# Performance work log

Measured on AMD Instinct MI355X. Metric: run time of the kernel, lower is better.

## Reference

```python
import jax, jax.numpy as jnp
import numpy as np

N, E, D, H, R = 100000, 1600000, 128, 128, 8


def rgcn_layer(x, W_rel, W_root, bias, src, dst, etype):
    """PyG-style RGCNConv: per-relation mean aggregation + root transform.

    out[i] = x[i] @ W_root + bias + sum_r mean_{j: (j->i, r)} x[j] @ W_rel[r]
    Mean commutes with the linear map, so we segment-mean raw features per
    (dst, relation) pair, then apply a single batched einsum.
    """
    n = x.shape[0]
    r = W_rel.shape[0]
    seg = dst * r + etype                                   # [E]
    msg = x[src]                                            # [E, D]
    agg = jax.ops.segment_sum(msg, seg, num_segments=n * r)  # [N*R, D]
    cnt = jax.ops.segment_sum(jnp.ones((msg.shape[0],), x.dtype), seg,
                              num_segments=n * r)
    agg = agg / jnp.maximum(cnt, 1.0)[:, None]              # per-relation mean
    agg = agg.reshape(n, r, -1)                             # [N, R, D]
    return jnp.einsum('nrd,rdh->nh', agg, W_rel) + x @ W_root + bias


def setup_inputs() -> dict:
    key = jax.random.key(0)
    ks = jax.random.split(key, 12)
    x = jax.random.normal(ks[0], (N, D), dtype=jnp.float32)
    edge_index = jax.random.randint(ks[1], (2, E), 0, N, dtype=jnp.int64)
    edge_type = jax.random.randint(ks[2], (E,), 0, R, dtype=jnp.int64)
    s = lambda fan_in: 1.0 / np.sqrt(fan_in)
    W_rel1 = jax.random.normal(ks[3], (R, D, H), dtype=jnp.float32) * s(D)
    W_root1 = jax.random.normal(ks[4], (D, H), dtype=jnp.float32) * s(D)
    b1 = jnp.zeros((H,), dtype=jnp.float32)
    W_rel2 = jax.random.normal(ks[5], (R, H, H), dtype=jnp.float32) * s(H)
    W_root2 = jax.random.normal(ks[6], (H, H), dtype=jnp.float32) * s(H)
    b2 = jnp.zeros((H,), dtype=jnp.float32)
    out_w = jax.random.normal(ks[7], (H, 1), dtype=jnp.float32) * s(H)
    out_b = jnp.zeros((1,), dtype=jnp.float32)
    return {"x": x, "edge_index": edge_index, "edge_type": edge_type,
            "W_rel1": W_rel1, "W_root1": W_root1, "b1": b1,
            "W_rel2": W_rel2, "W_root2": W_root2, "b2": b2,
            "out_w": out_w, "out_b": out_b}


def reference(x, edge_index, edge_type, W_rel1, W_root1, b1,
              W_rel2, W_root2, b2, out_w, out_b):
    src, dst = edge_index[0], edge_index[1]
    h = jax.nn.relu(rgcn_layer(x, W_rel1, W_root1, b1, src, dst, edge_type))
    h = jax.nn.relu(rgcn_layer(h, W_rel2, W_root2, b2, src, dst, edge_type))
    return jax.nn.sigmoid(h @ out_w + out_b).squeeze(-1)  # [N]
```

## Files before the change

### kernel.cpp

```cpp
#include <hip/hip_runtime.h>
#include <cstdint>
#include <cstddef>

#define NNODES 100000
#define NEDGES 1600000
#define DIM 128
#define NREL 8
#define QCAP 40
#define QI4 (QCAP / 4)
#define NKT 36
#define A16ROW 1160
#define NB 196
#define BCAP 9216
#define EPB 8192
#define BIN_BLKS ((NEDGES + EPB - 1) / EPB)
#define CVT4 (NNODES * DIM / 4)
#define CVT_BLKS (CVT4 / 1024)
#define PACK_UNITS (NKT * 8 * 2)
#define PACK_BLKS ((PACK_UNITS + 15) / 16)

typedef float f32x4 __attribute__((ext_vector_type(4)));
typedef float float8 __attribute__((ext_vector_type(8)));
typedef short short8 __attribute__((ext_vector_type(8)));
typedef _Float16 half8 __attribute__((ext_vector_type(8)));

__device__ inline unsigned short f2h(float f) {
    return __builtin_bit_cast(unsigned short, (_Float16)f);
}

__global__ __launch_bounds__(1024) void passA(const int* __restrict__ src,
                                              const int* __restrict__ dst,
                                              const int* __restrict__ et,
                                              int* __restrict__ gcur,
                                              int* __restrict__ qtmp,
                                              const float* __restrict__ x,
                                              unsigned short* __restrict__ xh,
                                              const float* __restrict__ Wrel1,
                                              const float* __restrict__ Wroot1,
                                              const float* __restrict__ Wrel2,
                                              const float* __restrict__ Wroot2,
                                              unsigned short* __restrict__ Wp1,
                                              unsigned short* __restrict__ Wp2) {
    int b = blockIdx.x;
    const int tid = threadIdx.x;
    if (b < BIN_BLKS) {
        __shared__ int cnt[NB];
        __shared__ int cur[NB];
        if (tid < NB) cnt[tid] = 0;
        __syncthreads();
        int ent[8], bkt[8];
        const int ebase = b * EPB + tid;
#pragma unroll
        for (int k = 0; k < 8; ++k) {
            int e = ebase + k * 1024;
            bkt[k] = -1;
            if (e < NEDGES) {
                int d = dst[e];
                int bb = d >> 9;
                bkt[k] = bb;
                ent[k] = src[e] | (et[e] << 17) | ((d & 511) << 20);
                atomicAdd(&cnt[bb], 1);
            }
        }
        __syncthreads();
        if (tid < NB) {
            int c = cnt[tid];
            cur[tid] = (c > 0) ? atomicAdd(&gcur[tid], c) : 0;
        }
        __syncthreads();
#pragma unroll
        for (int k = 0; k < 8; ++k) {
            if (bkt[k] >= 0) {
                int p = atomicAdd(&cur[bkt[k]], 1);
                if (p < BCAP) qtmp[(size_t)bkt[k] * BCAP + p] = ent[k];
            }
        }
        return;
    }
    b -= BIN_BLKS;
    if (b < CVT_BLKS) {
        int gid = b * 1024 + tid;
        float4 v = *(const float4*)(x + (size_t)gid * 4);
        ushort4 o = make_ushort4(f2h(v.x), f2h(v.y), f2h(v.z), f2h(v.w));
        *(ushort4*)(xh + (size_t)gid * 4) = o;
        return;
    }
    b -= CVT_BLKS;
    int unit = b * 16 + (tid >> 6);
    if (unit >= PACK_UNITS) return;
    int lane = tid & 63;
    int bb = unit;
    const float* Wrel = Wrel1;
    const float* Wroot = Wroot1;
    unsigned short* Wp = Wp1;
    if (bb >= NKT * 8) {
        bb -= NKT * 8;
        Wrel = Wrel2; Wroot = Wroot2; Wp = Wp2;
    }
    const int kt = bb >> 3, ht = bb & 7;
    const int col = ht * 16 + (lane & 15);
    const int kbase = kt * 32 + (lane >> 4) * 8;
    unsigned short vals[8];
#pragma unroll
    for (int j = 0; j < 8; ++j) {
        int k = kbase + j;
        float f = (k < 1024) ? Wrel[(size_t)k * 128 + col]
                             : Wroot[(size_t)(k - 1024) * 128 + col];
        vals[j] = f2h(f);
    }
    unsigned short* dstp = Wp + ((size_t)bb * 64 + lane) * 8;
#pragma unroll
    for (int j = 0; j < 8; ++j) dstp[j] = vals[j];
}

__global__ __launch_bounds__(1024) void passB(const int* __restrict__ qtmp,
                                              const int* __restrict__ gcur,
                                              int* __restrict__ fill,
                                              int* __restrict__ qlist) {
    const int b = blockIdx.x;
    const int tid = threadIdx.x;
    __shared__ int ncnt[512];
    if (tid < 512) ncnt[tid] = 0;
    __syncthreads();
    int total = gcur[b];
    if (total > BCAP) total = BCAP;
    int ent[9], loc[9];
#pragma unroll
    for (int k = 0; k < 9; ++k) {
        int i = tid + k * 1024;
        loc[k] = -1;
        if (i < total) {
            int e = qtmp[(size_t)b * BCAP + i];
            ent[k] = e;
            loc[k] = ((unsigned)e) >> 20;
            atomicAdd(&ncnt[loc[k]], 1);
        }
    }
    __syncthreads();
    if (tid < 512) {
        int n = b * 512 + tid;
        if (n < NNODES) fill[n] = ncnt[tid];
        ncnt[tid] = 0;
    }
    __syncthreads();
#pragma unroll
    for (int k = 0; k < 9; ++k) {
        if (loc[k] >= 0) {
            int p = atomicAdd(&ncnt[loc[k]], 1);
            if (p < QCAP) {
                int n = b * 512 + loc[k];
                int cv = (ent[k] & 0x1FFFF) | (((((unsigned)ent[k]) >> 17) & 7) << 20);
                qlist[(size_t)n * QCAP + p] = cv;
            }
        }
    }
}

#define FLUSH8 {                                                               \
    float sc = __shfl(invv, cur, 8);                                           \
    short8 o;                                                                  \
    _Pragma("unroll")                                                          \
    for (int j = 0; j < 8; ++j) o[j] = (short)f2h(accv[j] * sc);               \
    *(short8*)(Arow + cur * DIM + l16 * 8) = o;                                \
    accv = (float8){0.f, 0.f, 0.f, 0.f, 0.f, 0.f, 0.f, 0.f};                   \
}

__global__ __launch_bounds__(512, 4) void fused_layer(
    const unsigned short* __restrict__ feat,
    const int* __restrict__ fill,
    const int* __restrict__ qlist,
    const unsigned short* __restrict__ Wp,
    const float* __restrict__ bias,
    unsigned short* __restrict__ out,
    const float* __restrict__ outw,
    const float* __restrict__ outb,
    float* __restrict__ head_out) {
    __shared__ __align__(16) unsigned short A16[32 * A16ROW + 8];
    __shared__ int qs[32][QCAP];
    __shared__ int cnt[32][8];
    const int tid = threadIdx.x;
    const int blk = blockIdx.x;
    const int g = tid >> 4, l16 = tid & 15;

    const int n = blk * 32 + g;
    const int r8 = l16 & 7;

    const int fraw = fill[n];
    const int ecnt = fraw < QCAP ? fraw : QCAP;

    unsigned short* Arow = &A16[g * A16ROW];

    *(short8*)(Arow + 1024 + l16 * 8) =
        *(const short8*)(feat + (size_t)n * DIM + l16 * 8);

    if (l16 < 8) cnt[g][l16] = 0;
    int4 raw = make_int4(0, 0, 0, 0);
    if (l16 < QI4)
        raw = *(const int4*)(qlist + (size_t)n * QCAP + l16 * 4);
    __builtin_amdgcn_sched_barrier(0);
    {
        int vals[4] = {raw.x, raw.y, raw.z, raw.w};
        const int bidx = l16 * 4;
        if (l16 < QI4) {
#pragma unroll
            for (int j = 0; j < 4; ++j)
                if (bidx + j < ecnt)
                    atomicAdd(&cnt[g][((unsigned)vals[j]) >> 20], 1);
        }
        __builtin_amdgcn_sched_barrier(0);
        const int c = cnt[g][r8];
        const float invv_ = 1.0f / (float)(c > 1 ? c : 1);

#pragma unroll
        for (int r = 0; r < 8; ++r) {
            int cr = __shfl(c, r, 16);
            if (cr == 0) {
                short8 z = {0, 0, 0, 0, 0, 0, 0, 0};
                *(short8*)(Arow + r * DIM + l16 * 8) = z;
            }
        }

        int incl = c;
#pragma unroll
        for (int d1 = 1; d1 < 8; d1 <<= 1) {
            int u = __shfl_up(incl, d1, 8);
            if (r8 >= d1) incl += u;
        }
        if (l16 < 8) cnt[g][l16] = incl - c;
        __builtin_amdgcn_sched_barrier(0);
        if (l16 < QI4) {
#pragma unroll
            for (int j = 0; j < 4; ++j)
                if (bidx + j < ecnt) {
                    int rel = ((unsigned)vals[j]) >> 20;
                    int p = atomicAdd(&cnt[g][rel], 1);
                    qs[g][p] = vals[j];
                }
        }
        __builtin_amdgcn_sched_barrier(0);

        if (ecnt > 0) {
            const float invv = invv_;
            const int last = ecnt - 1;
            int q[8], qn[8];
            short8 v[8];
#pragma unroll
            for (int u = 0; u < 8; ++u) q[u] = qs[g][u < last ? u : last];
#pragma unroll
            for (int u = 0; u < 8; ++u)
                v[u] = *(const short8*)(feat +
                         (size_t)((unsigned)q[u] & 0xFFFFFu) * DIM + l16 * 8);

            float8 accv = {0.f, 0.f, 0.f, 0.f, 0.f, 0.f, 0.f, 0.f};
            int cur = ((unsigned)q[0]) >> 20;

            for (int e = 0; e < ecnt; e += 8) {
#pragma unroll
                for (int u = 0; u < 8; ++u) {
                    int p = e + 8 + u;
                    qn[u] = qs[g][p < last ? p : last];
                }
#pragma unroll
                for (int u = 0; u < 8; ++u) {
                    if (e + u < ecnt) {
                        const int s = ((unsigned)q[u]) >> 20;
                        if (s != cur) { FLUSH8 cur = s; }
                        accv += __builtin_convertvector(
                            __builtin_bit_cast(half8, v[u]), float8);
                    }
                }
#pragma unroll
                for (int u = 0; u < 8; ++u) {
                    v[u] = *(const short8*)(feat +
                             (size_t)((unsigned)qn[u] & 0xFFFFFu) * DIM + l16 * 8);
                    q[u] = qn[u];
                }
            }
            FLUSH8
        }
    }
    __syncthreads();

    const int lane = tid & 63;
    const int w = tid >> 6;
    const int m = lane & 15, kq = lane >> 4;
    const unsigned short* arow0 = &A16[m * A16ROW + kq * 8];
    const unsigned short* arow1 = &A16[(m + 16) * A16ROW + kq * 8];
    const unsigned short* bb = Wp + ((size_t)w * 64 + lane) * 8;

    f32x4 acc0 = {0.f, 0.f, 0.f, 0.f};
    f32x4 acc1 = {0.f, 0.f, 0.f, 0.f};
#pragma unroll 4
    for (int kt = 0; kt < NKT; ++kt) {
        short8 b0 = *(const short8*)(bb + (size_t)kt * 4096);
        short8 a0 = *(const short8*)(arow0 + kt * 32);
        short8 a1 = *(const short8*)(arow1 + kt * 32);
        acc0 = __builtin_amdgcn_mfma_f32_16x16x32_f16(
            __builtin_bit_cast(half8, a0), __builtin_bit_cast(half8, b0), acc0, 0, 0, 0);
        acc1 = __builtin_amdgcn_mfma_f32_16x16x32_f16(
            __builtin_bit_cast(half8, a1), __builtin_bit_cast(half8, b0), acc1, 0, 0, 0);
    }

    const int col = lane & 15;
    const int rbase = kq * 4;
    const int h0 = 16 * w + col;
    const float bv0 = bias[h0];

    if (!head_out) {
#pragma unroll
        for (int r = 0; r < 4; ++r) {
            const size_t nrow0 = ((size_t)blk * 32 + rbase + r) * DIM;
            const size_t nrow1 = ((size_t)blk * 32 + 16 + rbase + r) * DIM;
            out[nrow0 + h0] = f2h(fmaxf(acc0[r] + bv0, 0.f));
            out[nrow1 + h0] = f2h(fmaxf(acc1[r] + bv0, 0.f));
        }
    } else {
        const float w0 = outw[h0];
        float p0[4], p1[4];
#pragma unroll
        for (int r = 0; r < 4; ++r) {
            p0[r] = fmaxf(acc0[r] + bv0, 0.f) * w0;
            p1[r] = fmaxf(acc1[r] + bv0, 0.f) * w0;
#pragma unroll
            for (int d = 1; d < 16; d <<= 1) {
                p0[r] += __shfl_xor(p0[r], d, 16);
                p1[r] += __shfl_xor(p1[r], d, 16);
            }
        }
        __syncthreads();
        float* hp = (float*)A16;
        if (col == 0) {
#pragma unroll
            for (int r = 0; r < 4; ++r) {
                hp[(rbase + r) * 8 + w] = p0[r];
                hp[(16 + rbase + r) * 8 + w] = p1[r];
            }
        }
        __syncthreads();
        if (tid < 32) {
            float vsum = outb[0];
#pragma unroll
            for (int k = 0; k < 8; ++k) vsum += hp[tid * 8 + k];
            head_out[blk * 32 + tid] = 1.0f / (1.0f + __expf(-vsum));
        }
    }
}

extern "C" void kernel_launch(void* const* d_in, const int* in_sizes, int n_in,
                              void* d_out, int out_size, void* d_ws, size_t ws_size,
                              hipStream_t stream) {
    const float* x      = (const float*)d_in[0];
    const int*   ei     = (const int*)d_in[1];
    const int*   et     = (const int*)d_in[2];
    const float* Wrel1  = (const float*)d_in[3];
    const float* Wroot1 = (const float*)d_in[4];
    const float* b1     = (const float*)d_in[5];
    const float* Wrel2  = (const float*)d_in[6];
    const float* Wroot2 = (const float*)d_in[7];
    const float* b2     = (const float*)d_in[8];
    const float* outw   = (const float*)d_in[9];
    const float* outb   = (const float*)d_in[10];
    const int* src = ei;
    const int* dst = ei + NEDGES;

    char* ws = (char*)d_ws;
    int*            gcur   = (int*)(ws + 0);
    int*            qtmp   = (int*)(ws + 1024);
    int*            fill   = (int*)(ws + 7226368);
    int*            qlist  = (int*)(ws + 7626368);
    unsigned short* xh     = (unsigned short*)(ws + 23626368);
    unsigned short* h1     = (unsigned short*)(ws + 49226368);
    unsigned short* Wp1    = (unsigned short*)(ws + 74826368);
    unsigned short* Wp2    = (unsigned short*)(ws + 75121280);

    hipMemsetAsync(gcur, 0, 1024, stream);
    passA<<<BIN_BLKS + CVT_BLKS + PACK_BLKS, 1024, 0, stream>>>(
        src, dst, et, gcur, qtmp, x, xh,
        Wrel1, Wroot1, Wrel2, Wroot2, Wp1, Wp2);
    passB<<<NB, 1024, 0, stream>>>(qtmp, gcur, fill, qlist);

    fused_layer<<<NNODES / 32, 512, 0, stream>>>(xh, fill, qlist, Wp1, b1,
                                                 h1, nullptr, nullptr, nullptr);
    fused_layer<<<NNODES / 32, 512, 0, stream>>>(h1, fill, qlist, Wp2, b2,
                                                 nullptr, outw, outb, (float*)d_out);
}
```

Measured before the change: 360.2 us.

## Sort nodes by in-degree so each block processes similar-degree nodes

Builds a degree histogram in passB, scans it, and produces a permutation that groups nodes by in-degree. Both fused layers then map each block's 32 rows through this permutation and scatter outputs back, so the 16-lane groups in a block have similar gather loop trip counts and less divergence and tail imbalance. The inner accumulation also becomes branchless, multiplying by a 0/1 mask instead of skipping. In exchange it adds two small kernels, atomic contention on the histogram, and scattered output writes. Neighbour gathers for a block are also no longer for consecutive nodes.

```diff
diff --git a/kernel.cpp b/kernel.cpp
--- a/kernel.cpp
+++ b/kernel.cpp
@@ -18,6 +18,7 @@
 #define CVT_BLKS (CVT4 / 1024)
 #define PACK_UNITS (NKT * 8 * 2)
 #define PACK_BLKS ((PACK_UNITS + 15) / 16)
+#define NDEG 41
 
 typedef float f32x4 __attribute__((ext_vector_type(4)));
 typedef float float8 __attribute__((ext_vector_type(8)));
@@ -116,7 +117,8 @@
 __global__ __launch_bounds__(1024) void passB(const int* __restrict__ qtmp,
                                               const int* __restrict__ gcur,
                                               int* __restrict__ fill,
-                                              int* __restrict__ qlist) {
+                                              int* __restrict__ qlist,
+                                              int* __restrict__ dhist) {
     const int b = blockIdx.x;
     const int tid = threadIdx.x;
     __shared__ int ncnt[512];
@@ -139,7 +141,11 @@
     __syncthreads();
     if (tid < 512) {
         int n = b * 512 + tid;
-        if (n < NNODES) fill[n] = ncnt[tid];
+        if (n < NNODES) {
+            int c = ncnt[tid];
+            fill[n] = c;
+            atomicAdd(&dhist[c < (NDEG - 1) ? c : (NDEG - 1)], 1);
+        }
         ncnt[tid] = 0;
     }
     __syncthreads();
@@ -156,6 +162,29 @@
     }
 }
 
+__global__ __launch_bounds__(64) void dscan(const int* __restrict__ dhist,
+                                            int* __restrict__ dcur) {
+    int lane = threadIdx.x;
+    int v = (lane < NDEG) ? dhist[lane] : 0;
+    int incl = v;
+    for (int d = 1; d < 64; d <<= 1) {
+        int u = __shfl_up(incl, d);
+        if (lane >= d) incl += u;
+    }
+    if (lane < NDEG) dcur[lane] = incl - v;
+}
+
+__global__ __launch_bounds__(1024) void assign_perm(const int* __restrict__ fill,
+                                                    int* __restrict__ dcur,
+                                                    int* __restrict__ perm) {
+    int n = blockIdx.x * 1024 + threadIdx.x;
+    if (n >= NNODES) return;
+    int c = fill[n];
+    c = c < (NDEG - 1) ? c : (NDEG - 1);
+    int p = atomicAdd(&dcur[c], 1);
+    perm[p] = n;
+}
+
 #define FLUSH8 {                                                               \
     float sc = __shfl(invv, cur, 8);                                           \
     short8 o;                                                                  \
@@ -169,6 +198,7 @@
     const unsigned short* __restrict__ feat,
     const int* __restrict__ fill,
     const int* __restrict__ qlist,
+    const int* __restrict__ perm,
     const unsigned short* __restrict__ Wp,
     const float* __restrict__ bias,
     unsigned short* __restrict__ out,
@@ -178,12 +208,14 @@
     __shared__ __align__(16) unsigned short A16[32 * A16ROW + 8];
     __shared__ int qs[32][QCAP];
     __shared__ int cnt[32][8];
+    __shared__ int pnode[32];
     const int tid = threadIdx.x;
     const int blk = blockIdx.x;
     const int g = tid >> 4, l16 = tid & 15;
 
-    const int n = blk * 32 + g;
+    const int n = perm[blk * 32 + g];
     const int r8 = l16 & 7;
+    if (l16 == 0) pnode[g] = n;
 
     const int fraw = fill[n];
     const int ecnt = fraw < QCAP ? fraw : QCAP;
@@ -262,12 +294,13 @@
                 }
 #pragma unroll
                 for (int u = 0; u < 8; ++u) {
-                    if (e + u < ecnt) {
-                        const int s = ((unsigned)q[u]) >> 20;
-                        if (s != cur) { FLUSH8 cur = s; }
-                        accv += __builtin_convertvector(
-                            __builtin_bit_cast(half8, v[u]), float8);
-                    }
+                    const int s = ((unsigned)q[u]) >> 20;
+                    if (s != cur) { FLUSH8 cur = s; }
+                    const half8 hv = __builtin_bit_cast(half8, v[u]);
+                    const float mml = (e + u < ecnt) ? 1.0f : 0.0f;
+#pragma unroll
+                    for (int k = 0; k < 8; ++k)
+                        accv[k] = fmaf((float)hv[k], mml, accv[k]);
                 }
 #pragma unroll
                 for (int u = 0; u < 8; ++u) {
@@ -309,10 +342,10 @@
     if (!head_out) {
 #pragma unroll
         for (int r = 0; r < 4; ++r) {
-            const size_t nrow0 = ((size_t)blk * 32 + rbase + r) * DIM;
-            const size_t nrow1 = ((size_t)blk * 32 + 16 + rbase + r) * DIM;
-            out[nrow0 + h0] = f2h(fmaxf(acc0[r] + bv0, 0.f));
-            out[nrow1 + h0] = f2h(fmaxf(acc1[r] + bv0, 0.f));
+            const size_t n0 = (size_t)pnode[rbase + r] * DIM;
+            const size_t n1 = (size_t)pnode[16 + rbase + r] * DIM;
+            out[n0 + h0] = f2h(fmaxf(acc0[r] + bv0, 0.f));
+            out[n1 + h0] = f2h(fmaxf(acc1[r] + bv0, 0.f));
         }
     } else {
         const float w0 = outw[h0];
@@ -341,7 +374,7 @@
             float vsum = outb[0];
 #pragma unroll
             for (int k = 0; k < 8; ++k) vsum += hp[tid * 8 + k];
-            head_out[blk * 32 + tid] = 1.0f / (1.0f + __expf(-vsum));
+            head_out[pnode[tid]] = 1.0f / (1.0f + __expf(-vsum));
         }
     }
 }
@@ -365,22 +398,27 @@
 
     char* ws = (char*)d_ws;
     int*            gcur   = (int*)(ws + 0);
-    int*            qtmp   = (int*)(ws + 1024);
-    int*            fill   = (int*)(ws + 7226368);
-    int*            qlist  = (int*)(ws + 7626368);
-    unsigned short* xh     = (unsigned short*)(ws + 23626368);
-    unsigned short* h1     = (unsigned short*)(ws + 49226368);
-    unsigned short* Wp1    = (unsigned short*)(ws + 74826368);
-    unsigned short* Wp2    = (unsigned short*)(ws + 75121280);
-
-    hipMemsetAsync(gcur, 0, 1024, stream);
+    int*            dhist  = (int*)(ws + 1024);
+    int*            dcur   = (int*)(ws + 2048);
+    int*            perm   = (int*)(ws + 3072);
+    int*            qtmp   = (int*)(ws + 403072);
+    int*            fill   = (int*)(ws + 7628416);
+    int*            qlist  = (int*)(ws + 8028416);
+    unsigned short* xh     = (unsigned short*)(ws + 24028416);
+    unsigned short* h1     = (unsigned short*)(ws + 49628416);
+    unsigned short* Wp1    = (unsigned short*)(ws + 75228416);
+    unsigned short* Wp2    = (unsigned short*)(ws + 75523328);
+
+    hipMemsetAsync(gcur, 0, 2048, stream);
     passA<<<BIN_BLKS + CVT_BLKS + PACK_BLKS, 1024, 0, stream>>>(
         src, dst, et, gcur, qtmp, x, xh,
         Wrel1, Wroot1, Wrel2, Wroot2, Wp1, Wp2);
-    passB<<<NB, 1024, 0, stream>>>(qtmp, gcur, fill, qlist);
-
-    fused_layer<<<NNODES / 32, 512, 0, stream>>>(xh, fill, qlist, Wp1, b1,
+    passB<<<NB, 1024, 0, stream>>>(qtmp, gcur, fill, qlist, dhist);
+    dscan<<<1, 64, 0, stream>>>(dhist, dcur);
+    assign_perm<<<(NNODES + 1023) / 1024, 1024, 0, stream>>>(fill, dcur, perm);
+
+    fused_layer<<<NNODES / 32, 512, 0, stream>>>(xh, fill, qlist, perm, Wp1, b1,
                                                  h1, nullptr, nullptr, nullptr);
-    fused_layer<<<NNODES / 32, 512, 0, stream>>>(h1, fill, qlist, Wp2, b2,
+    fused_layer<<<NNODES / 32, 512, 0, stream>>>(h1, fill, qlist, perm, Wp2, b2,
                                                  nullptr, outw, outb, (float*)d_out);
 }
```

New measurement: 875.7 us. 2.43x slower.

## Sort nodes by degree within block, per-wave binning histograms, branchless accumulate

Applied to the files above, without the earlier changes.

Within each fused_layer block, the 32 nodes are ranked by edge count so that nodes with similar degree land in the same wavefront, which cuts divergence in the gather loop. Outputs are remapped through the permutation. The binning pass now keeps a separate shared histogram per wave, which reduces contention on shared-memory atomics. The inner accumulate is made branchless with a 0/1 mask FMA. These add an extra barrier, a rank computation and unconditional flush checks on padded entries.

```diff
diff --git a/kernel.cpp b/kernel.cpp
--- a/kernel.cpp
+++ b/kernel.cpp
@@ -18,6 +18,7 @@
 #define CVT_BLKS (CVT4 / 1024)
 #define PACK_UNITS (NKT * 8 * 2)
 #define PACK_BLKS ((PACK_UNITS + 15) / 16)
+#define NWAVE 16
 
 typedef float f32x4 __attribute__((ext_vector_type(4)));
 typedef float float8 __attribute__((ext_vector_type(8)));
@@ -44,9 +45,9 @@
     int b = blockIdx.x;
     const int tid = threadIdx.x;
     if (b < BIN_BLKS) {
-        __shared__ int cnt[NB];
-        __shared__ int cur[NB];
-        if (tid < NB) cnt[tid] = 0;
+        __shared__ int whist[NWAVE][NB];
+        const int wv = tid >> 6;
+        for (int i = tid; i < NWAVE * NB; i += 1024) ((int*)whist)[i] = 0;
         __syncthreads();
         int ent[8], bkt[8];
         const int ebase = b * EPB + tid;
@@ -59,19 +60,27 @@
                 int bb = d >> 9;
                 bkt[k] = bb;
                 ent[k] = src[e] | (et[e] << 17) | ((d & 511) << 20);
-                atomicAdd(&cnt[bb], 1);
+                atomicAdd(&whist[wv][bb], 1);
             }
         }
         __syncthreads();
         if (tid < NB) {
-            int c = cnt[tid];
-            cur[tid] = (c > 0) ? atomicAdd(&gcur[tid], c) : 0;
+            int tot = 0;
+#pragma unroll
+            for (int w = 0; w < NWAVE; ++w) tot += whist[w][tid];
+            int run = (tot > 0) ? atomicAdd(&gcur[tid], tot) : 0;
+#pragma unroll
+            for (int w = 0; w < NWAVE; ++w) {
+                int c = whist[w][tid];
+                whist[w][tid] = run;
+                run += c;
+            }
         }
         __syncthreads();
 #pragma unroll
         for (int k = 0; k < 8; ++k) {
             if (bkt[k] >= 0) {
-                int p = atomicAdd(&cur[bkt[k]], 1);
+                int p = atomicAdd(&whist[wv][bkt[k]], 1);
                 if (p < BCAP) qtmp[(size_t)bkt[k] * BCAP + p] = ent[k];
             }
         }
@@ -178,14 +187,29 @@
     __shared__ __align__(16) unsigned short A16[32 * A16ROW + 8];
     __shared__ int qs[32][QCAP];
     __shared__ int cnt[32][8];
+    __shared__ int pnode[32];
+    __shared__ int pcnt[32];
     const int tid = threadIdx.x;
     const int blk = blockIdx.x;
     const int g = tid >> 4, l16 = tid & 15;
 
-    const int n = blk * 32 + g;
+    if (tid < 32) {
+        const int nn = blk * 32 + tid;
+        const int c = fill[nn];
+        int rank = 0;
+#pragma unroll
+        for (int j = 0; j < 32; ++j) {
+            int cj = __shfl(c, j, 32);
+            if ((cj > c) || (cj == c && j < tid)) ++rank;
+        }
+        pnode[rank] = nn;
+        pcnt[rank] = c;
+    }
+    __syncthreads();
+
+    const int n = pnode[g];
+    const int fraw = pcnt[g];
     const int r8 = l16 & 7;
-
-    const int fraw = fill[n];
     const int ecnt = fraw < QCAP ? fraw : QCAP;
 
     unsigned short* Arow = &A16[g * A16ROW];
@@ -262,12 +286,13 @@
                 }
 #pragma unroll
                 for (int u = 0; u < 8; ++u) {
-                    if (e + u < ecnt) {
-                        const int s = ((unsigned)q[u]) >> 20;
-                        if (s != cur) { FLUSH8 cur = s; }
-                        accv += __builtin_convertvector(
-                            __builtin_bit_cast(half8, v[u]), float8);
-                    }
+                    const int s = ((unsigned)q[u]) >> 20;
+                    if (s != cur) { FLUSH8 cur = s; }
+                    const half8 hv = __builtin_bit_cast(half8, v[u]);
+                    const float mml = (e + u < ecnt) ? 1.0f : 0.0f;
+#pragma unroll
+                    for (int k = 0; k < 8; ++k)
+                        accv[k] = fmaf((float)hv[k], mml, accv[k]);
                 }
 #pragma unroll
                 for (int u = 0; u < 8; ++u) {
@@ -309,10 +334,10 @@
     if (!head_out) {
 #pragma unroll
         for (int r = 0; r < 4; ++r) {
-            const size_t nrow0 = ((size_t)blk * 32 + rbase + r) * DIM;
-            const size_t nrow1 = ((size_t)blk * 32 + 16 + rbase + r) * DIM;
-            out[nrow0 + h0] = f2h(fmaxf(acc0[r] + bv0, 0.f));
-            out[nrow1 + h0] = f2h(fmaxf(acc1[r] + bv0, 0.f));
+            const size_t n0 = (size_t)pnode[rbase + r] * DIM;
+            const size_t n1 = (size_t)pnode[16 + rbase + r] * DIM;
+            out[n0 + h0] = f2h(fmaxf(acc0[r] + bv0, 0.f));
+            out[n1 + h0] = f2h(fmaxf(acc1[r] + bv0, 0.f));
         }
     } else {
         const float w0 = outw[h0];
@@ -341,7 +366,7 @@
             float vsum = outb[0];
 #pragma unroll
             for (int k = 0; k < 8; ++k) vsum += hp[tid * 8 + k];
-            head_out[blk * 32 + tid] = 1.0f / (1.0f + __expf(-vsum));
+            head_out[pnode[tid]] = 1.0f / (1.0f + __expf(-vsum));
         }
     }
 }
```

New measurement: 380.3 us. 1.06x slower.
